# Kernel tuning notes

Measured on AMD Instinct MI355X. Metric: run time of the kernel, lower is better.

The kernel has to match this reference:

```python
import jax, jax.numpy as jnp
import numpy as np

EPS = 1e-5
NUM_HEADS = 8
BLOCK_SIZE = 8


def _ln(x, w, b):
    mu = jnp.mean(x, axis=-1, keepdims=True)
    var = jnp.mean((x - mu) ** 2, axis=-1, keepdims=True)
    return (x - mu) * jax.lax.rsqrt(var + EPS) * w + b


def _mha(x, wqkv, bqkv, wo, bo, allowed):
    # x: [b,t,d]; wqkv: [3d,d]; allowed: [t,t] bool (True = attend)
    b, t, d = x.shape
    h, hd = NUM_HEADS, d // NUM_HEADS
    qkv = x @ wqkv.T + bqkv
    q, k, v = jnp.split(qkv, 3, axis=-1)
    q = q.reshape(b, t, h, hd)
    k = k.reshape(b, t, h, hd)
    v = v.reshape(b, t, h, hd)
    scores = jnp.einsum('bihd,bjhd->bhij', q, k) / np.sqrt(hd).astype(x.dtype)
    scores = jnp.where(allowed[None, None], scores, -jnp.inf)
    attn = jax.nn.softmax(scores, axis=-1)
    out = jnp.einsum('bhij,bjhd->bihd', attn, v).reshape(b, t, d)
    return out @ wo.T + bo


def setup_inputs() -> dict:
    key = jax.random.key(0)
    ks = jax.random.split(key, 20)
    B, T, D, FF, L, MAXT = 64, 512, 256, 512, 4, 512
    s = 0.02
    return {
        'latents': jax.random.normal(ks[0], (B, T, D), dtype=jnp.float32),
        'move_ids': jax.random.randint(ks[1], (B, T), 0, 20480),
        'mask': jax.random.randint(ks[2], (B, T), 0, 2).astype(bool),
        'positional': s * jax.random.normal(ks[3], (1, MAXT, D), dtype=jnp.float32),
        'embed_from': s * jax.random.normal(ks[4], (64, D), dtype=jnp.float32),
        'embed_to': s * jax.random.normal(ks[5], (64, D), dtype=jnp.float32),
        'embed_promo': s * jax.random.normal(ks[6], (5, D), dtype=jnp.float32),
        'in_proj_w': s * jax.random.normal(ks[7], (L, 3 * D, D), dtype=jnp.float32),
        'in_proj_b': jnp.zeros((L, 3 * D), dtype=jnp.float32),
        'out_w': s * jax.random.normal(ks[8], (L, D, D), dtype=jnp.float32),
        'out_b': jnp.zeros((L, D), dtype=jnp.float32),
        'fc1_w': s * jax.random.normal(ks[9], (L, FF, D), dtype=jnp.float32),
        'fc1_b': jnp.zeros((L, FF), dtype=jnp.float32),
        'fc2_w': s * jax.random.normal(ks[10], (L, D, FF), dtype=jnp.float32),
        'fc2_b': jnp.zeros((L, D), dtype=jnp.float32),
        'norm_w': jnp.ones((D,), dtype=jnp.float32),
        'norm_b': jnp.zeros((D,), dtype=jnp.float32),
    }


def reference(latents, move_ids, mask, positional, embed_from, embed_to,
              embed_promo, in_proj_w, in_proj_b, out_w, out_b,
              fc1_w, fc1_b, fc2_w, fc2_b, norm_w, norm_b):
    b, t, d = latents.shape
    # move-id decomposition: promo/from/to embedding sum
    promo = move_ids // 4096
    rem = move_ids % 4096
    frm = rem // 64
    to = rem % 64
    x = latents + positional[:, :t, :] + embed_from[frm] + embed_to[to] + embed_promo[promo]
    # block-causal mask: token i may attend j iff block(j) <= block(i)
    bidx = jnp.arange(t) // BLOCK_SIZE
    allowed = bidx[None, :] <= bidx[:, None]
    n_layers = in_proj_w.shape[0]
    for l in range(n_layers):
        # NOTE: the single LayerNorm (norm_w, norm_b) is shared everywhere,
        # exactly as in the original module.
        x = x + _mha(_ln(x, norm_w, norm_b), in_proj_w[l], in_proj_b[l],
                     out_w[l], out_b[l], allowed)
        h1 = jax.nn.relu(_ln(x, norm_w, norm_b) @ fc1_w[l].T + fc1_b[l])
        x = x + h1 @ fc2_w[l].T + fc2_b[l]
    x = _ln(x, norm_w, norm_b)
    return jnp.where(mask[..., None], x, latents)
```

## Files before the change

### kernel.cpp

```cpp
#include <hip/hip_runtime.h>
#include <math.h>

#define Bv  64
#define Tv  512
#define Dv  256
#define FFv 512
#define Lv  4
#define BTv (Bv*Tv)
#define EPSv 1e-5f
#define QSC 0.25509402f

typedef __attribute__((ext_vector_type(8))) short short8;
typedef __attribute__((ext_vector_type(4))) float f32x4;
typedef unsigned short us;

#if __has_builtin(__builtin_amdgcn_exp2f)
#define EXP2(x) __builtin_amdgcn_exp2f(x)
#else
#define EXP2(x) exp2f(x)
#endif

#define WAITV(n) asm volatile("s_waitcnt vmcnt(" #n ")" ::: "memory")

__device__ __forceinline__ us f2bf(float f) {
    unsigned r;
    asm("v_cvt_pk_bf16_f32 %0, %1, 0" : "=v"(r) : "v"(f));
    return (us)r;
}
__device__ __forceinline__ unsigned pk2(float a, float b) {
    unsigned r;
    asm("v_cvt_pk_bf16_f32 %0, %1, %2" : "=v"(r) : "v"(a), "v"(b));
    return r;
}
__device__ __forceinline__ float wave_sum(float v) {
#pragma unroll
    for (int o = 32; o > 0; o >>= 1) v += __shfl_xor(v, o);
    return v;
}

__global__ __launch_bounds__(256) void cvtall_kernel(
    const float* __restrict__ qw, const float* __restrict__ ow,
    const float* __restrict__ f1, const float* __restrict__ f2,
    const float* __restrict__ qb,
    us* __restrict__ wq, us* __restrict__ wo, us* __restrict__ w1,
    us* __restrict__ w2, float* __restrict__ sb)
{
    int blk = blockIdx.x, tid = threadIdx.x;
    if (blk < 2048) {
        const float* s; us* d; int i; float sc = 1.0f;
        if (blk < 768)       { i = blk*256 + tid;        s = qw; d = wq;
                               sc = (((i >> 6) % 768) < 256) ? QSC : 1.0f; }
        else if (blk < 1024) { i = (blk-768)*256 + tid;  s = ow; d = wo; }
        else if (blk < 1536) { i = (blk-1024)*256 + tid; s = f1; d = w1; }
        else                 { i = (blk-1536)*256 + tid; s = f2; d = w2; }
        float4 v = ((const float4*)s)[i];
        uint2 o;
        o.x = pk2(v.x*sc, v.y*sc);
        o.y = pk2(v.z*sc, v.w*sc);
        ((uint2*)d)[i] = o;
    } else {
        int i = (blk-2048)*256 + tid;
        sb[i] = qb[i] * (((i % 768) < 256) ? QSC : 1.0f);
    }
}

__global__ __launch_bounds__(256) void embed_ln_kernel(
    const float* __restrict__ lat, const int* __restrict__ mids,
    const float* __restrict__ pos, const float* __restrict__ ef,
    const float* __restrict__ et,  const float* __restrict__ ep,
    const float* __restrict__ nw,  const float* __restrict__ nb,
    float* __restrict__ x, us* __restrict__ xn)
{
    int wv = threadIdx.x >> 6, lane = threadIdx.x & 63;
    size_t row = (size_t)blockIdx.x * 4 + wv;
    int t  = (int)(row & (Tv - 1));
    int id = mids[row];
    int promo = id >> 12;
    int rem   = id & 4095;
    int frm   = rem >> 6;
    int to    = rem & 63;
    float4 v  = ((const float4*)(lat + row*Dv))[lane];
    float4 pv = ((const float4*)(pos + (size_t)t*Dv))[lane];
    float4 fv = ((const float4*)(ef + (size_t)frm*Dv))[lane];
    float4 tv = ((const float4*)(et + (size_t)to*Dv))[lane];
    float4 ev = ((const float4*)(ep + (size_t)promo*Dv))[lane];
    v.x += pv.x + fv.x + tv.x + ev.x;
    v.y += pv.y + fv.y + tv.y + ev.y;
    v.z += pv.z + fv.z + tv.z + ev.z;
    v.w += pv.w + fv.w + tv.w + ev.w;
    ((float4*)(x + row*Dv))[lane] = v;
    float mu = wave_sum(v.x + v.y + v.z + v.w) * (1.0f/Dv);
    float dx = v.x-mu, dy = v.y-mu, dz = v.z-mu, dw = v.w-mu;
    float var = wave_sum(dx*dx + dy*dy + dz*dz + dw*dw) * (1.0f/Dv);
    float inv = rsqrtf(var + EPSv);
    float4 w4 = ((const float4*)nw)[lane];
    float4 b4 = ((const float4*)nb)[lane];
    uint2 o;
    o.x = pk2(dx*inv*w4.x + b4.x, dy*inv*w4.y + b4.y);
    o.y = pk2(dz*inv*w4.z + b4.z, dw*inv*w4.w + b4.w);
    ((uint2*)(xn + row*Dv))[lane] = o;
}

__global__ __launch_bounds__(256) void final_kernel(
    const float* __restrict__ x, const float* __restrict__ lat,
    const int* __restrict__ mask, const float* __restrict__ w,
    const float* __restrict__ b, float* __restrict__ out)
{
    int wv = threadIdx.x >> 6, lane = threadIdx.x & 63;
    size_t row = (size_t)blockIdx.x * 4 + wv;
    float4 v = ((const float4*)(x + row*Dv))[lane];
    float mu = wave_sum(v.x + v.y + v.z + v.w) * (1.0f/Dv);
    float dx = v.x-mu, dy = v.y-mu, dz = v.z-mu, dw = v.w-mu;
    float var = wave_sum(dx*dx + dy*dy + dz*dz + dw*dw) * (1.0f/Dv);
    float inv = rsqrtf(var + EPSv);
    float4 w4 = ((const float4*)w)[lane];
    float4 b4 = ((const float4*)b)[lane];
    float4 o;
    o.x = dx*inv*w4.x + b4.x;
    o.y = dy*inv*w4.y + b4.y;
    o.z = dz*inv*w4.z + b4.z;
    o.w = dw*inv*w4.w + b4.w;
    if (!mask[row]) o = ((const float4*)(lat + row*Dv))[lane];
    ((float4*)(out + row*Dv))[lane] = o;
}

template<int RELU>
__global__ __launch_bounds__(256) void mm_kernel(
    const us* __restrict__ A, const us* __restrict__ B,
    const float* __restrict__ bias, us* __restrict__ C,
    int M, int N, int K)
{
    __shared__ us As[2][128*64];
    __shared__ us Bs[2][128*64];
    int tid  = threadIdx.x;
    int lane = tid & 63;
    int wu   = __builtin_amdgcn_readfirstlane(tid >> 6);
    int m0 = blockIdx.x * 128, n0 = blockIdx.y * 128;
    int wm = wu & 1, wn = wu >> 1;
    f32x4 acc[4][4] = {};
    int srow = lane >> 3;
    int sg   = (lane & 7) ^ srow;
    const us* Ag = A + (size_t)m0 * K + sg*8;
    const us* Bg = B + (size_t)n0 * K + sg*8;
    int cc = lane & 15, q4 = lane >> 4;

#define STG(kk, bb) { \
    _Pragma("unroll") \
    for (int p = 0; p < 4; p++) { \
        int row = wu*32 + p*8; \
        __builtin_amdgcn_global_load_lds( \
            (const __attribute__((address_space(1))) unsigned int*)(Ag + (size_t)(row + srow)*K + (kk)), \
            (__attribute__((address_space(3))) unsigned int*)(&As[bb][row*64]), \
            16, 0, 0); \
        __builtin_amdgcn_global_load_lds( \
            (const __attribute__((address_space(1))) unsigned int*)(Bg + (size_t)(row + srow)*K + (kk)), \
            (__attribute__((address_space(3))) unsigned int*)(&Bs[bb][row*64]), \
            16, 0, 0); \
    } }

    int nk = K >> 6;
    STG(0, 0);
    if (nk > 1) STG(64, 1);
    int cur = 0;
    for (int t = 0; t < nk; t++) {
        if (t < nk - 1) { WAITV(8); } else { WAITV(0); }
        __builtin_amdgcn_s_barrier();
        __builtin_amdgcn_sched_barrier(0);
#pragma unroll
        for (int h = 0; h < 2; h++) {
            int pg = ((h*4 + q4) ^ (cc & 7)) * 8;
            short8 av[4], bv[4];
#pragma unroll
            for (int i = 0; i < 4; i++)
                av[i] = *(const short8*)(&As[cur][(wm*64 + i*16 + cc)*64 + pg]);
#pragma unroll
            for (int j = 0; j < 4; j++)
                bv[j] = *(const short8*)(&Bs[cur][(wn*64 + j*16 + cc)*64 + pg]);
#pragma unroll
            for (int i = 0; i < 4; i++)
#pragma unroll
                for (int j = 0; j < 4; j++)
                    acc[i][j] = __builtin_amdgcn_mfma_f32_16x16x32_bf16(av[i], bv[j], acc[i][j], 0, 0, 0);
        }
        __builtin_amdgcn_sched_barrier(0);
        __builtin_amdgcn_s_barrier();
        __builtin_amdgcn_sched_barrier(0);
        if (t + 2 < nk) STG((t+2)*64, cur);
        cur ^= 1;
    }
#undef STG
#pragma unroll
    for (int j = 0; j < 4; j++) {
        int n = n0 + wn*64 + j*16 + cc;
        float bj = bias[n];
#pragma unroll
        for (int i = 0; i < 4; i++) {
#pragma unroll
            for (int r = 0; r < 4; r++) {
                int m = m0 + wm*64 + i*16 + q4*4 + r;
                float v = acc[i][j][r] + bj;
                if (RELU) v = fmaxf(v, 0.f);
                C[(size_t)m * N + n] = f2bf(v);
            }
        }
    }
}

__global__ __launch_bounds__(512) void mmfuse_kernel(
    const us* __restrict__ A, const us* __restrict__ B,
    const float* __restrict__ bias, float* __restrict__ x,
    us* __restrict__ xn, const float* __restrict__ nw,
    const float* __restrict__ nb, int M, int K)
{
    __shared__ us As[2][128*64];
    __shared__ us Bs[2][256*64];
    __shared__ float red[128][4][2];
    __shared__ float mus[128], rss[128];
    int tid  = threadIdx.x;
    int lane = tid & 63;
    int wu   = __builtin_amdgcn_readfirstlane(tid >> 6);
    int m0 = blockIdx.x * 128;
    int wm = wu & 1, wn = wu >> 1;
    f32x4 acc[4][4] = {};
    int srow = lane >> 3;
    int sg   = (lane & 7) ^ srow;
    const us* Ag = A + (size_t)m0 * K + sg*8;
    const us* Bg = B + sg*8;
    int cc = lane & 15, q4 = lane >> 4;

#define STG(kk, bb) { \
    _Pragma("unroll") \
    for (int p = 0; p < 2; p++) { \
        int row = wu*16 + p*8; \
        __builtin_amdgcn_global_load_lds( \
            (const __attribute__((address_space(1))) unsigned int*)(Ag + (size_t)(row + srow)*K + (kk)), \
            (__attribute__((address_space(3))) unsigned int*)(&As[bb][row*64]), \
            16, 0, 0); \
    } \
    _Pragma("unroll") \
    for (int p = 0; p < 4; p++) { \
        int row = wu*32 + p*8; \
        __builtin_amdgcn_global_load_lds( \
            (const __attribute__((address_space(1))) unsigned int*)(Bg + (size_t)(row + srow)*K + (kk)), \
            (__attribute__((address_space(3))) unsigned int*)(&Bs[bb][row*64]), \
            16, 0, 0); \
    } }

    int nk = K >> 6;
    STG(0, 0);
    if (nk > 1) STG(64, 1);
    int cur = 0;
    for (int t = 0; t < nk; t++) {
        if (t < nk - 1) { WAITV(6); } else { WAITV(0); }
        __builtin_amdgcn_s_barrier();
        __builtin_amdgcn_sched_barrier(0);
#pragma unroll
        for (int h = 0; h < 2; h++) {
            int pg = ((h*4 + q4) ^ (cc & 7)) * 8;
            short8 av[4], bv[4];
#pragma unroll
            for (int i = 0; i < 4; i++)
                av[i] = *(const short8*)(&As[cur][(wm*64 + i*16 + cc)*64 + pg]);
#pragma unroll
            for (int j = 0; j < 4; j++)
                bv[j] = *(const short8*)(&Bs[cur][(wn*64 + j*16 + cc)*64 + pg]);
#pragma unroll
            for (int i = 0; i < 4; i++)
#pragma unroll
                for (int j = 0; j < 4; j++)
                    acc[i][j] = __builtin_amdgcn_mfma_f32_16x16x32_bf16(av[i], bv[j], acc[i][j], 0, 0, 0);
        }
        __builtin_amdgcn_sched_barrier(0);
        __builtin_amdgcn_s_barrier();
        __builtin_amdgcn_sched_barrier(0);
        if (t + 2 < nk) STG((t+2)*64, cur);
        cur ^= 1;
    }
#undef STG

    float bb4[4], nwv[4], nbv[4];
#pragma unroll
    for (int j = 0; j < 4; j++) {
        int n = wn*64 + j*16 + cc;
        bb4[j] = bias[n]; nwv[j] = nw[n]; nbv[j] = nb[n];
    }
#pragma unroll
    for (int i = 0; i < 4; i++) {
        float s[4] = {0.f,0.f,0.f,0.f}, sq[4] = {0.f,0.f,0.f,0.f};
#pragma unroll
        for (int j = 0; j < 4; j++) {
#pragma unroll
            for (int r = 0; r < 4; r++) {
                int ml = wm*64 + i*16 + q4*4 + r;
                size_t off = (size_t)(m0 + ml) * Dv + wn*64 + j*16 + cc;
                float v = acc[i][j][r] + bb4[j] + x[off];
                acc[i][j][r] = v;
                x[off] = v;
                s[r] += v; sq[r] += v*v;
            }
        }
#pragma unroll
        for (int r = 0; r < 4; r++) {
#pragma unroll
            for (int o = 1; o < 16; o <<= 1) {
                s[r]  += __shfl_xor(s[r],  o);
                sq[r] += __shfl_xor(sq[r], o);
            }
        }
        if (cc == 0) {
#pragma unroll
            for (int r = 0; r < 4; r++) {
                red[wm*64 + i*16 + q4*4 + r][wn][0] = s[r];
                red[wm*64 + i*16 + q4*4 + r][wn][1] = sq[r];
            }
        }
    }
    __syncthreads();
    if (tid < 128) {
        float ts = red[tid][0][0] + red[tid][1][0] + red[tid][2][0] + red[tid][3][0];
        float tq = red[tid][0][1] + red[tid][1][1] + red[tid][2][1] + red[tid][3][1];
        float mu = ts * (1.0f/Dv);
        float var = tq * (1.0f/Dv) - mu*mu;
        mus[tid] = mu;
        rss[tid] = rsqrtf(var + EPSv);
    }
    __syncthreads();
#pragma unroll
    for (int i = 0; i < 4; i++) {
#pragma unroll
        for (int r = 0; r < 4; r++) {
            int ml = wm*64 + i*16 + q4*4 + r;
            float mu = mus[ml], rv = rss[ml];
#pragma unroll
            for (int j = 0; j < 4; j++) {
                size_t off = (size_t)(m0 + ml) * Dv + wn*64 + j*16 + cc;
                xn[off] = f2bf((acc[i][j][r] - mu)*rv*nwv[j] + nbv[j]);
            }
        }
    }
}

__global__ __launch_bounds__(256) void attn_kernel(
    const us* __restrict__ qkv, us* __restrict__ ao)
{
    int blk = blockIdx.x;
    int b  = blk & 63;
    int h  = (blk >> 6) & 7;
    int qt = blk >> 9;
    int i0 = qt << 6;
    int tid = threadIdx.x;
    int lane = tid & 63;
    int wu = tid >> 6;

    __shared__ us Ks[2][64][40];
    __shared__ us Vt[2][32][72];
    __shared__ us Ps[4][16][72];
    __shared__ float Ls[4][16];

    size_t rowbase = (size_t)b * Tv;
    int c = lane & 15, q4 = lane >> 4;

    short8 qfrag = *(const short8*)(qkv + (rowbase + i0 + wu*16 + c)*768 + h*32 + q4*8);

    int skey = tid >> 2, sdc = (tid & 3) << 3;
    int vkey = tid & 63, vg = tid >> 6;
    const us* kgp = qkv + (rowbase + skey)*768 + 256 + h*32 + sdc;
    const us* vgp = qkv + (rowbase + vkey)*768 + 512 + h*32 + vg*8;

    f32x4 oacc[2] = {};
    float lsum = 0.f;
    int ntiles = qt + 1;

    short8 kreg = *(const short8*)(kgp);
    short8 vreg = *(const short8*)(vgp);
    *(short8*)&Ks[0][skey][sdc] = kreg;
#pragma unroll
    for (int j = 0; j < 8; j++) Vt[0][vg*8 + j][vkey] = vreg[j];
    if (ntiles > 1) {
        kreg = *(const short8*)(kgp + 64*768);
        vreg = *(const short8*)(vgp + 64*768);
    }
    __syncthreads();

    for (int kt = 0; kt < ntiles; kt++) {
        int cur = kt & 1;
        if (kt + 1 < ntiles) {
            *(short8*)&Ks[cur^1][skey][sdc] = kreg;
#pragma unroll
            for (int j = 0; j < 8; j++) Vt[cur^1][vg*8 + j][vkey] = vreg[j];
        }
        if (kt + 2 < ntiles) {
            kreg = *(const short8*)(kgp + (size_t)(kt+2)*64*768);
            vreg = *(const short8*)(vgp + (size_t)(kt+2)*64*768);
        }

        f32x4 st[4];
#pragma unroll
        for (int jt = 0; jt < 4; jt++) {
            short8 kf = *(const short8*)&Ks[cur][jt*16 + c][q4*8];
            st[jt] = __builtin_amdgcn_mfma_f32_16x16x32_bf16(kf, qfrag, (f32x4){0.f,0.f,0.f,0.f}, 0, 0, 0);
        }
        bool diag = (kt == ntiles - 1);
#pragma unroll
        for (int jt = 0; jt < 4; jt++) {
            float msk = (!diag || (2*jt + (q4 >> 1) <= 2*wu + (c >> 3))) ? 1.f : 0.f;
            float p0 = EXP2(st[jt][0]) * msk;
            float p1 = EXP2(st[jt][1]) * msk;
            float p2 = EXP2(st[jt][2]) * msk;
            float p3 = EXP2(st[jt][3]) * msk;
            lsum += p0 + p1 + p2 + p3;
            uint2 w2; w2.x = pk2(p0, p1); w2.y = pk2(p2, p3);
            *(uint2*)&Ps[wu][c][jt*16 + q4*4] = w2;
        }
#pragma unroll
        for (int kk = 0; kk < 2; kk++) {
            short8 pf = *(const short8*)&Ps[wu][c][kk*32 + q4*8];
#pragma unroll
            for (int dt = 0; dt < 2; dt++) {
                short8 vf = *(const short8*)&Vt[cur][dt*16 + c][kk*32 + q4*8];
                oacc[dt] = __builtin_amdgcn_mfma_f32_16x16x32_bf16(pf, vf, oacc[dt], 0, 0, 0);
            }
        }
        __syncthreads();
    }

    float l = lsum;
    l += __shfl_xor(l, 16);
    l += __shfl_xor(l, 32);
    if (q4 == 0) Ls[wu][c] = 1.0f / l;
    float4 lv4 = *(const float4*)&Ls[wu][q4*4];
#pragma unroll
    for (int dt = 0; dt < 2; dt++) {
#pragma unroll
        for (int r = 0; r < 4; r++) {
            float li = (r == 0) ? lv4.x : (r == 1) ? lv4.y : (r == 2) ? lv4.z : lv4.w;
            ao[(rowbase + i0 + wu*16 + q4*4 + r)*256 + h*32 + dt*16 + c] = f2bf(oacc[dt][r] * li);
        }
    }
}

extern "C" void kernel_launch(void* const* d_in, const int* in_sizes, int n_in,
                              void* d_out, int out_size, void* d_ws, size_t ws_size,
                              hipStream_t stream)
{
    const float* latents    = (const float*)d_in[0];
    const int*   move_ids   = (const int*)  d_in[1];
    const int*   mask       = (const int*)  d_in[2];
    const float* positional = (const float*)d_in[3];
    const float* embed_from = (const float*)d_in[4];
    const float* embed_to   = (const float*)d_in[5];
    const float* embed_promo= (const float*)d_in[6];
    const float* in_proj_w  = (const float*)d_in[7];
    const float* in_proj_b  = (const float*)d_in[8];
    const float* out_w      = (const float*)d_in[9];
    const float* out_b      = (const float*)d_in[10];
    const float* fc1_w      = (const float*)d_in[11];
    const float* fc1_b      = (const float*)d_in[12];
    const float* fc2_w      = (const float*)d_in[13];
    const float* fc2_b      = (const float*)d_in[14];
    const float* norm_w     = (const float*)d_in[15];
    const float* norm_b     = (const float*)d_in[16];
    float* out = (float*)d_out;

    float* x   = (float*)d_ws;
    float* sb  = x + (size_t)BTv * Dv;
    us* xn  = (us*)(sb + Lv*768);
    us* qkv = xn + (size_t)BTv * Dv;
    us* ao  = qkv + (size_t)BTv * 768;
    us* h1  = ao + (size_t)BTv * Dv;
    us* wq  = h1 + (size_t)BTv * FFv;
    us* wo  = wq + (size_t)Lv * 768 * Dv;
    us* w1  = wo + (size_t)Lv * Dv * Dv;
    us* w2  = w1 + (size_t)Lv * FFv * Dv;

    cvtall_kernel<<<2060, 256, 0, stream>>>(in_proj_w, out_w, fc1_w, fc2_w,
                                            in_proj_b, wq, wo, w1, w2, sb);

    embed_ln_kernel<<<BTv/4, 256, 0, stream>>>(latents, move_ids, positional,
        embed_from, embed_to, embed_promo, norm_w, norm_b, x, xn);

    for (int l = 0; l < Lv; l++) {
        mm_kernel<0><<<dim3(BTv/128, 768/128), 256, 0, stream>>>(
            xn, wq + (size_t)l*768*Dv, sb + l*768, qkv, BTv, 768, Dv);
        attn_kernel<<<Bv*8*(Tv/64), 256, 0, stream>>>(qkv, ao);
        mmfuse_kernel<<<BTv/128, 512, 0, stream>>>(
            ao, wo + (size_t)l*Dv*Dv, out_b + l*Dv, x, xn, norm_w, norm_b,
            BTv, Dv);
        mm_kernel<1><<<dim3(BTv/128, FFv/128), 256, 0, stream>>>(
            xn, w1 + (size_t)l*FFv*Dv, fc1_b + l*FFv, h1, BTv, FFv, Dv);
        mmfuse_kernel<<<BTv/128, 512, 0, stream>>>(
            h1, w2 + (size_t)l*Dv*FFv, fc2_b + l*Dv, x, xn, norm_w, norm_b,
            BTv, FFv);
    }
    final_kernel<<<BTv/4, 256, 0, stream>>>(x, latents, mask, norm_w, norm_b, out);
}
```

Before: 621.0 us.

## Stage GEMM epilogue through LDS for coalesced stores; skip masked diagonal attention tiles

The GEMM epilogue now writes bf16 results into the reused LDS staging buffers and then copies full 128-column rows to global memory with 16-byte vector stores. This replaces the scattered 2-byte strided stores and adds one extra barrier. In the attention kernel, the diagonal K tile now skips QK MFMAs, exp work and PV MFMAs for sub-tiles that are fully masked, writing zeros into P instead. That saves compute on the last tile per query block, at the cost of added branching.

New measurement: 678.0 us. 9.2% more time.

```diff
diff --git a/kernel.cpp b/kernel.cpp
--- a/kernel.cpp
+++ b/kernel.cpp
@@ -189,20 +189,31 @@
         cur ^= 1;
     }
 #undef STG
-#pragma unroll
-    for (int j = 0; j < 4; j++) {
-        int n = n0 + wn*64 + j*16 + cc;
-        float bj = bias[n];
-#pragma unroll
-        for (int i = 0; i < 4; i++) {
-#pragma unroll
-            for (int r = 0; r < 4; r++) {
-                int m = m0 + wm*64 + i*16 + q4*4 + r;
-                float v = acc[i][j][r] + bj;
-                if (RELU) v = fmaxf(v, 0.f);
-                C[(size_t)m * N + n] = f2bf(v);
-            }
-        }
+
+    {
+        us* Cs = wm ? &Bs[0][0] : &As[0][0];
+#pragma unroll
+        for (int j = 0; j < 4; j++) {
+            int n = wn*64 + j*16 + cc;
+            float bj = bias[n0 + n];
+#pragma unroll
+            for (int i = 0; i < 4; i++) {
+#pragma unroll
+                for (int r = 0; r < 4; r++) {
+                    float v = acc[i][j][r] + bj;
+                    if (RELU) v = fmaxf(v, 0.f);
+                    Cs[(i*16 + q4*4 + r)*132 + n] = f2bf(v);
+                }
+            }
+        }
+        __syncthreads();
+        int row = tid >> 1, half = tid & 1;
+        const us* src = (row < 64 ? &As[0][0] + row*132
+                                  : &Bs[0][0] + (row - 64)*132) + half*64;
+        us* dst = C + (size_t)(m0 + row) * N + n0 + half*64;
+#pragma unroll
+        for (int k = 0; k < 8; k++)
+            *(short8*)(dst + k*8) = *(const short8*)(src + k*8);
     }
 }
 
@@ -394,31 +405,42 @@
             vreg = *(const short8*)(vgp + (size_t)(kt+2)*64*768);
         }
 
+        bool diag = (kt == ntiles - 1);
+        int jtend = diag ? (wu + 1) : 4;
         f32x4 st[4];
 #pragma unroll
         for (int jt = 0; jt < 4; jt++) {
-            short8 kf = *(const short8*)&Ks[cur][jt*16 + c][q4*8];
-            st[jt] = __builtin_amdgcn_mfma_f32_16x16x32_bf16(kf, qfrag, (f32x4){0.f,0.f,0.f,0.f}, 0, 0, 0);
-        }
-        bool diag = (kt == ntiles - 1);
+            if (jt < jtend) {
+                short8 kf = *(const short8*)&Ks[cur][jt*16 + c][q4*8];
+                st[jt] = __builtin_amdgcn_mfma_f32_16x16x32_bf16(kf, qfrag, (f32x4){0.f,0.f,0.f,0.f}, 0, 0, 0);
+            }
+        }
 #pragma unroll
         for (int jt = 0; jt < 4; jt++) {
-            float msk = (!diag || (2*jt + (q4 >> 1) <= 2*wu + (c >> 3))) ? 1.f : 0.f;
-            float p0 = EXP2(st[jt][0]) * msk;
-            float p1 = EXP2(st[jt][1]) * msk;
-            float p2 = EXP2(st[jt][2]) * msk;
-            float p3 = EXP2(st[jt][3]) * msk;
-            lsum += p0 + p1 + p2 + p3;
-            uint2 w2; w2.x = pk2(p0, p1); w2.y = pk2(p2, p3);
-            *(uint2*)&Ps[wu][c][jt*16 + q4*4] = w2;
-        }
+            if (jt < jtend) {
+                float msk = (diag && jt == wu) ? (((q4 >> 1) <= (c >> 3)) ? 1.f : 0.f) : 1.f;
+                float p0 = EXP2(st[jt][0]) * msk;
+                float p1 = EXP2(st[jt][1]) * msk;
+                float p2 = EXP2(st[jt][2]) * msk;
+                float p3 = EXP2(st[jt][3]) * msk;
+                lsum += p0 + p1 + p2 + p3;
+                uint2 w2; w2.x = pk2(p0, p1); w2.y = pk2(p2, p3);
+                *(uint2*)&Ps[wu][c][jt*16 + q4*4] = w2;
+            } else {
+                uint2 z; z.x = 0u; z.y = 0u;
+                *(uint2*)&Ps[wu][c][jt*16 + q4*4] = z;
+            }
+        }
+        int kkend = (diag && wu < 2) ? 1 : 2;
 #pragma unroll
         for (int kk = 0; kk < 2; kk++) {
-            short8 pf = *(const short8*)&Ps[wu][c][kk*32 + q4*8];
-#pragma unroll
-            for (int dt = 0; dt < 2; dt++) {
-                short8 vf = *(const short8*)&Vt[cur][dt*16 + c][kk*32 + q4*8];
-                oacc[dt] = __builtin_amdgcn_mfma_f32_16x16x32_bf16(pf, vf, oacc[dt], 0, 0, 0);
+            if (kk < kkend) {
+                short8 pf = *(const short8*)&Ps[wu][c][kk*32 + q4*8];
+#pragma unroll
+                for (int dt = 0; dt < 2; dt++) {
+                    short8 vf = *(const short8*)&Vt[cur][dt*16 + c][kk*32 + q4*8];
+                    oacc[dt] = __builtin_amdgcn_mfma_f32_16x16x32_bf16(pf, vf, oacc[dt], 0, 0, 0);
+                }
             }
         }
         __syncthreads();
```
